# Kernel optimization log

Hardware: AMD Instinct MI355X
Metric: run time of the kernel (lower is better)

## Reference

```python
import jax, jax.numpy as jnp
import numpy as np
import math

VOCAB, D, L, H, DFF, S, B = 32000, 1024, 6, 16, 4096, 512, 4
DK = D // H
EPS = 1e-6


def layernorm(x, g, b):
    # Faithful to source: divides by (std + eps), std is population std (unbiased=False)
    mu = jnp.mean(x, axis=-1, keepdims=True)
    std = jnp.sqrt(jnp.mean((x - mu) ** 2, axis=-1, keepdims=True))
    return g * (x - mu) / (std + EPS) + b


def setup_inputs() -> dict:
    key = jax.random.key(0)
    ks = jax.random.split(key, 12)
    s = 0.02
    inp = {
        "tokens": jax.random.randint(ks[0], (B, S), 0, VOCAB, dtype=jnp.int32),
        "tok_emb": jax.random.normal(ks[1], (VOCAB, D), jnp.float32) * s,
        "pos_emb": jax.random.normal(ks[2], (1, S, D), jnp.float32) * s,
        # per-layer stacked params [L, ...]
        "Wq": jax.random.normal(ks[3], (L, D, D), jnp.float32) * s,
        "bq": jnp.zeros((L, D), jnp.float32),
        "Wk": jax.random.normal(ks[4], (L, D, D), jnp.float32) * s,
        "bk": jnp.zeros((L, D), jnp.float32),
        "Wv": jax.random.normal(ks[5], (L, D, D), jnp.float32) * s,
        "bv": jnp.zeros((L, D), jnp.float32),
        "Wo": jax.random.normal(ks[6], (L, D, D), jnp.float32) * s,
        "bo": jnp.zeros((L, D), jnp.float32),
        "g1": jnp.ones((L, D), jnp.float32),
        "be1": jnp.zeros((L, D), jnp.float32),
        "W1": jax.random.normal(ks[7], (L, D, DFF), jnp.float32) * s,
        "bf1": jnp.zeros((L, DFF), jnp.float32),
        "W2": jax.random.normal(ks[8], (L, DFF, D), jnp.float32) * s,
        "bf2": jnp.zeros((L, D), jnp.float32),
        "g2": jnp.ones((L, D), jnp.float32),
        "be2": jnp.zeros((L, D), jnp.float32),
        "gf": jnp.ones((D,), jnp.float32),
        "bf": jnp.zeros((D,), jnp.float32),
    }
    return inp


def gpt_forward(tokens, tok_emb, pos_emb, Wq, bq, Wk, bk, Wv, bv, Wo, bo,
                g1, be1, W1, bf1, W2, bf2, g2, be2, gf, bf):
    seq = tokens.shape[1]
    x = tok_emb[tokens] * math.sqrt(D) + pos_emb[:, :seq, :]  # [B,S,D]
    causal = jnp.tril(jnp.ones((seq, seq), bool))  # [S,S]

    def block(x, p):
        wq, bq_, wk, bk_, wv, bv_, wo, bo_, g1_, be1_, w1, bf1_, w2, bf2_, g2_, be2_ = p
        h = layernorm(x, g1_, be1_)
        q = (h @ wq + bq_).reshape(B, seq, H, DK).transpose(0, 2, 1, 3)  # [B,H,S,DK]
        k = (h @ wk + bk_).reshape(B, seq, H, DK).transpose(0, 2, 1, 3)
        v = (h @ wv + bv_).reshape(B, seq, H, DK).transpose(0, 2, 1, 3)
        scores = jnp.einsum("bhqd,bhkd->bhqk", q, k) / math.sqrt(DK)
        scores = jnp.where(causal, scores, -1e9)
        p_attn = jax.nn.softmax(scores, axis=-1)
        attn = jnp.einsum("bhqk,bhkd->bhqd", p_attn, v)
        attn = attn.transpose(0, 2, 1, 3).reshape(B, seq, D)
        x = x + (attn @ wo + bo_)
        h2 = layernorm(x, g2_, be2_)
        ff = jnp.maximum(h2 @ w1 + bf1_, 0.0) @ w2 + bf2_
        return x + ff, None

    params = (Wq, bq, Wk, bk, Wv, bv, Wo, bo, g1, be1, W1, bf1, W2, bf2, g2, be2)
    x, _ = jax.lax.scan(block, x, params)
    x = layernorm(x, gf, bf)
    logits = x @ tok_emb.T  # tied head, no bias
    return logits


def reference(tokens, tok_emb, pos_emb, Wq, bq, Wk, bk, Wv, bv, Wo, bo,
              g1, be1, W1, bf1, W2, bf2, g2, be2, gf, bf):
    return gpt_forward(tokens, tok_emb, pos_emb, Wq, bq, Wk, bk, Wv, bv, Wo, bo,
                       g1, be1, W1, bf1, W2, bf2, g2, be2, gf, bf)
```

## Files before the change

kernel.cpp:

```cpp
#include <hip/hip_runtime.h>

#define TOKENS 2048
#define DM 1024
#define NHEAD 16
#define DH 64
#define SEQL 512
#define NBATCH 4
#define DFFN 4096
#define NLAYER 6
#define NVOCAB 32000

typedef short short8 __attribute__((ext_vector_type(8)));
typedef short short4v __attribute__((ext_vector_type(4)));
typedef float floatx4 __attribute__((ext_vector_type(4)));

#define FLAG_RELU 1
#define FLAG_OUTBF16 2

#define AS1 __attribute__((address_space(1)))
#define AS3 __attribute__((address_space(3)))

__device__ __forceinline__ float bf2f(short s) {
  unsigned u = ((unsigned)(unsigned short)s) << 16;
  return __builtin_bit_cast(float, u);
}
__device__ __forceinline__ short f2bf(float f) {
  unsigned u = __builtin_bit_cast(unsigned, f);
  u = (u + 0x7FFFu + ((u >> 16) & 1u)) >> 16;
  return (short)(unsigned short)u;
}

template<int N> __device__ __forceinline__ void wait_vm() {
  if constexpr (N == 0)      asm volatile("s_waitcnt vmcnt(0)" ::: "memory");
  else if constexpr (N == 3) asm volatile("s_waitcnt vmcnt(3)" ::: "memory");
  else if constexpr (N == 4) asm volatile("s_waitcnt vmcnt(4)" ::: "memory");
  else if constexpr (N == 6) asm volatile("s_waitcnt vmcnt(6)" ::: "memory");
  else if constexpr (N == 8) asm volatile("s_waitcnt vmcnt(8)" ::: "memory");
  else static_assert(N == 0, "unsupported vmcnt");
}

template<int BM, int BN, int WR, int WC, int BK>
__global__ __launch_bounds__(256) void gemm_db(
    const short* __restrict__ A, const short* __restrict__ Bt, void* __restrict__ Cv,
    const float* __restrict__ bias, const float* __restrict__ resid,
    int K, int lda, int ldb, int ldc, float alpha, int flags)
{
  constexpr int FI = BM / WR / 16;
  constexpr int FJ = BN / WC / 16;
  constexpr int RPI = (BK == 64) ? 32 : 64;
  constexpr int NST = BM / RPI + BN / RPI;
  __shared__ short As[2][BM * BK];
  __shared__ short Bs[2][BN * BK];

  const int gy = gridDim.y;
  int lin = blockIdx.x + gridDim.x * blockIdx.y;
  const int nwg = gridDim.x * gy;
  if ((nwg & 7) == 0) { const int cpx = nwg >> 3; lin = (lin & 7) * cpx + (lin >> 3); }
  const int row0 = (lin % gy) * BM, col0 = (lin / gy) * BN;

  const int tid = threadIdx.x;
  const int lane = tid & 63;
  const int wid = tid >> 6;
  const int wr = wid / WC, wc = wid % WC;
  const int lc = lane & 15, g = lane >> 4;
  const int sr = (BK == 64) ? (tid >> 3) : (tid >> 2);
  const int sc = (BK == 64) ? (tid & 7) : (tid & 3);
  const int swz_s = (BK == 64) ? (sr & 7) : ((sr >> 1) & 3);
  const int scs = (sc ^ swz_s) * 8;

  floatx4 acc[FI][FJ];
  #pragma unroll
  for (int i = 0; i < FI; ++i)
    #pragma unroll
    for (int j = 0; j < FJ; ++j)
      acc[i][j] = (floatx4){0.f, 0.f, 0.f, 0.f};

  auto stage = [&](int k0, int b) {
    char* ad = (char*)As[b];
    char* bd = (char*)Bs[b];
    #pragma unroll
    for (int it = 0; it < BM / RPI; ++it) {
      const short* src = A + (long)(row0 + it * RPI + sr) * lda + k0 + scs;
      __builtin_amdgcn_global_load_lds((const AS1 void*)src,
          (AS3 void*)(ad + it * 4096 + tid * 16), 16, 0, 0);
    }
    #pragma unroll
    for (int it = 0; it < BN / RPI; ++it) {
      const short* src = Bt + (long)(col0 + it * RPI + sr) * ldb + k0 + scs;
      __builtin_amdgcn_global_load_lds((const AS1 void*)src,
          (AS3 void*)(bd + it * 4096 + tid * 16), 16, 0, 0);
    }
  };

  const int NT = K / BK;
  stage(0, 0);
  int cb = 0;
  for (int t = 0; t < NT; ++t) {
    __builtin_amdgcn_s_barrier();
    __builtin_amdgcn_sched_barrier(0);
    if (t + 1 < NT) {
      stage((t + 1) * BK, cb ^ 1);
      wait_vm<NST>();
    } else {
      wait_vm<0>();
    }
    __builtin_amdgcn_sched_barrier(0);

    const short* as = As[cb];
    const short* bs = Bs[cb];
    if constexpr (BK == 64) {
      short8 fa[FI][2], fb[FJ][2];
      #pragma unroll
      for (int i = 0; i < FI; ++i) {
        const int r = wr * (BM / WR) + i * 16 + lc;
        fa[i][0] = *(const short8*)&as[r * 64 + ((g ^ (r & 7)) * 8)];
        fa[i][1] = *(const short8*)&as[r * 64 + (((4 + g) ^ (r & 7)) * 8)];
      }
      #pragma unroll
      for (int j = 0; j < FJ; ++j) {
        const int r = wc * (BN / WC) + j * 16 + lc;
        fb[j][0] = *(const short8*)&bs[r * 64 + ((g ^ (r & 7)) * 8)];
        fb[j][1] = *(const short8*)&bs[r * 64 + (((4 + g) ^ (r & 7)) * 8)];
      }
      #pragma unroll
      for (int i = 0; i < FI; ++i)
        #pragma unroll
        for (int j = 0; j < FJ; ++j) {
          acc[i][j] = __builtin_amdgcn_mfma_f32_16x16x32_bf16(fa[i][0], fb[j][0], acc[i][j], 0, 0, 0);
          acc[i][j] = __builtin_amdgcn_mfma_f32_16x16x32_bf16(fa[i][1], fb[j][1], acc[i][j], 0, 0, 0);
        }
    } else {
      short8 fa[FI], fb[FJ];
      #pragma unroll
      for (int i = 0; i < FI; ++i) {
        const int r = wr * (BM / WR) + i * 16 + lc;
        fa[i] = *(const short8*)&as[r * 32 + ((g ^ ((r >> 1) & 3)) * 8)];
      }
      #pragma unroll
      for (int j = 0; j < FJ; ++j) {
        const int r = wc * (BN / WC) + j * 16 + lc;
        fb[j] = *(const short8*)&bs[r * 32 + ((g ^ ((r >> 1) & 3)) * 8)];
      }
      #pragma unroll
      for (int i = 0; i < FI; ++i)
        #pragma unroll
        for (int j = 0; j < FJ; ++j)
          acc[i][j] = __builtin_amdgcn_mfma_f32_16x16x32_bf16(fa[i], fb[j], acc[i][j], 0, 0, 0);
    }
    cb ^= 1;
  }

  const bool relu = flags & FLAG_RELU;
  const bool obf  = flags & FLAG_OUTBF16;
  float* Cf = (float*)Cv;
  short* Cb = (short*)Cv;
  #pragma unroll
  for (int i = 0; i < FI; ++i) {
    int orow = row0 + wr * (BM / WR) + i * 16 + g * 4;
    #pragma unroll
    for (int j = 0; j < FJ; ++j) {
      int ocol = col0 + wc * (BN / WC) + j * 16 + lc;
      #pragma unroll
      for (int t = 0; t < 4; ++t) {
        long off = (long)(orow + t) * ldc + ocol;
        float v = alpha * acc[i][j][t];
        if (bias)  v += bias[ocol];
        if (resid) v += resid[off];
        if (relu)  v = fmaxf(v, 0.f);
        if (obf) Cb[off] = f2bf(v); else Cf[off] = v;
      }
    }
  }
}

template<int BM, int BN, int WR, int WC, int BK>
static inline void launch_gemm(hipStream_t st, const short* A, const short* Bt, void* C,
    const float* bias, const float* resid, int M, int N, int K,
    int lda, int ldb, int ldc, float alpha, int flags)
{
  dim3 grid(N / BN, M / BM, 1), blk(256);
  gemm_db<BM, BN, WR, WC, BK><<<grid, blk, 0, st>>>(A, Bt, C, bias, resid,
                                                    K, lda, ldb, ldc, alpha, flags);
}

__global__ __launch_bounds__(512, 2) void gemm256p(
    const short* __restrict__ A, const short* __restrict__ Bt, float* __restrict__ C,
    int K, int lda, int ldb, int ldc)
{
  __shared__ short As[2][2][128 * 64];
  __shared__ short Bs[2][4][64 * 64];

  const int gy = gridDim.y;
  int lin = blockIdx.x + gridDim.x * blockIdx.y;
  const int nwg = gridDim.x * gy;
  if ((nwg & 7) == 0) { const int cpx = nwg >> 3; lin = (lin & 7) * cpx + (lin >> 3); }
  const int row0 = (lin % gy) * 256, col0 = (lin / gy) * 256;

  const int tid = threadIdx.x;
  const int lane = tid & 63;
  const int w = tid >> 6;
  const int wr = w >> 2, wc = w & 3;
  const int lc = lane & 15, g = lane >> 4;
  const int sr = tid >> 3;
  const int sc = tid & 7;
  const int scs = (sc ^ (sr & 7)) * 8;

  floatx4 acc[8][4];
  #pragma unroll
  for (int i = 0; i < 8; ++i)
    #pragma unroll
    for (int j = 0; j < 4; ++j)
      acc[i][j] = (floatx4){0.f, 0.f, 0.f, 0.f};

  auto stageA = [&](int k0, int b, int h) {
    #pragma unroll
    for (int it = 0; it < 2; ++it) {
      const int r = h * 128 + it * 64 + sr;
      const short* src = A + (long)(row0 + r) * lda + k0 + scs;
      __builtin_amdgcn_global_load_lds((const AS1 void*)src,
          (AS3 void*)((char*)&As[b][h][0] + it * 8192 + tid * 16), 16, 0, 0);
    }
  };
  auto stageBq = [&](int k0, int b, int q) {
    const short* src = Bt + (long)(col0 + q * 64 + sr) * ldb + k0 + scs;
    __builtin_amdgcn_global_load_lds((const AS1 void*)src,
        (AS3 void*)((char*)&Bs[b][q][0] + tid * 16), 16, 0, 0);
  };
  auto rdA = [&](int b, int sub, short8 fa[4][2]) {
    const short* base = &As[b][wr][0];
    #pragma unroll
    for (int i = 0; i < 4; ++i) {
      const int r = sub * 64 + i * 16 + lc;
      fa[i][0] = *(const short8*)&base[r * 64 + ((g ^ (r & 7)) * 8)];
      fa[i][1] = *(const short8*)&base[r * 64 + (((4 + g) ^ (r & 7)) * 8)];
    }
  };
  auto rdB = [&](int b, int sub, short8 fb[2][2]) {
    const short* base = &Bs[b][wc][0];
    #pragma unroll
    for (int j = 0; j < 2; ++j) {
      const int r = sub * 32 + j * 16 + lc;
      fb[j][0] = *(const short8*)&base[r * 64 + ((g ^ (r & 7)) * 8)];
      fb[j][1] = *(const short8*)&base[r * 64 + (((4 + g) ^ (r & 7)) * 8)];
    }
  };
  auto mm = [&](short8 fa[4][2], short8 fb[2][2], int io, int jo) {
    #pragma unroll
    for (int i = 0; i < 4; ++i)
      #pragma unroll
      for (int j = 0; j < 2; ++j) {
        floatx4 c = acc[io + i][jo + j];
        c = __builtin_amdgcn_mfma_f32_16x16x32_bf16(fa[i][0], fb[j][0], c, 0, 0, 0);
        c = __builtin_amdgcn_mfma_f32_16x16x32_bf16(fa[i][1], fb[j][1], c, 0, 0, 0);
        acc[io + i][jo + j] = c;
      }
  };

#define PH_SYNC() \
    __builtin_amdgcn_s_barrier(); \
    asm volatile("s_waitcnt lgkmcnt(0)" ::: "memory"); \
    __builtin_amdgcn_sched_barrier(0); \
    __builtin_amdgcn_s_setprio(1);
#define PH_END() \
    __builtin_amdgcn_s_setprio(0); \
    __builtin_amdgcn_s_barrier();

  const int NT = K >> 6;
  stageA(0, 0, 0); stageA(0, 0, 1);
  stageBq(0, 0, 0); stageBq(0, 0, 1); stageBq(0, 0, 2); stageBq(0, 0, 3);
  stageA(64, 1, 0); stageA(64, 1, 1);
  wait_vm<4>();
  __builtin_amdgcn_s_barrier();

  for (int t = 0; t < NT; ++t) {
    const int b = t & 1;
    const int nk = (t + 1) << 6;
    short8 fa[4][2], fb0[2][2], fb1[2][2];
    rdA(b, 0, fa); rdB(b, 0, fb0);
    if (t + 1 < NT) { stageBq(nk, b ^ 1, 0); stageBq(nk, b ^ 1, 1); }
    PH_SYNC();
    mm(fa, fb0, 0, 0);
    PH_END();
    rdB(b, 1, fb1);
    if (t + 1 < NT) { stageBq(nk, b ^ 1, 2); stageBq(nk, b ^ 1, 3); }
    PH_SYNC();
    mm(fa, fb1, 0, 2);
    PH_END();
    rdA(b, 1, fa);
    PH_SYNC();
    mm(fa, fb1, 4, 2);
    PH_END();
    if (t + 2 < NT) {
      stageA((t + 2) << 6, b, 0); stageA((t + 2) << 6, b, 1);
      wait_vm<4>();
    } else {
      wait_vm<0>();
    }
    __builtin_amdgcn_sched_barrier(0);
    __builtin_amdgcn_s_barrier();
    __builtin_amdgcn_s_setprio(1);
    mm(fa, fb0, 4, 0);
    PH_END();
  }
#undef PH_SYNC
#undef PH_END

  #pragma unroll
  for (int i = 0; i < 8; ++i) {
    int orow = row0 + wr * 128 + i * 16 + g * 4;
    #pragma unroll
    for (int j = 0; j < 4; ++j) {
      int ocol = col0 + wc * 64 + j * 16 + lc;
      #pragma unroll
      for (int t = 0; t < 4; ++t)
        C[(long)(orow + t) * ldc + ocol] = acc[i][j][t];
    }
  }
}

__global__ __launch_bounds__(256) void flash_attn(
    const short* __restrict__ qkv, const short* __restrict__ Vt,
    short* __restrict__ attn)
{
  const int qt = blockIdx.x;
  const int bh = blockIdx.y;
  const int b = bh >> 4, h = bh & 15;
  const int row0 = qt * 64;

  __shared__ short Kt[64 * 64];
  __shared__ short Vtl[64 * 64];
  __shared__ short Pt[4 * 16 * 64];

  const int tid = threadIdx.x;
  const int lane = tid & 63;
  const int wid = tid >> 6;
  const int lc = lane & 15, g = lane >> 4;

  short8 qf[2];
  {
    const short* qp = qkv + (long)(b * SEQL + row0 + wid * 16 + lc) * 3072 + h * DH;
    qf[0] = *(const short8*)(qp + g * 8);
    qf[1] = *(const short8*)(qp + 32 + g * 8);
  }

  floatx4 o[4];
  float m[4], l[4];
  #pragma unroll
  for (int j = 0; j < 4; ++j) o[j] = (floatx4){0.f, 0.f, 0.f, 0.f};
  #pragma unroll
  for (int t = 0; t < 4; ++t) { m[t] = -3e38f; l[t] = 0.f; }

  for (int kv0 = 0; kv0 <= row0; kv0 += 64) {
    #pragma unroll
    for (int i = 0; i < 2; ++i) {
      const int idx = i * 256 + tid;
      const int r = idx >> 3, cc = idx & 7;
      const int sw = cc ^ (r & 7);
      const short* ks = qkv + (long)(b * SEQL + kv0 + r) * 3072 + 1024 + h * DH + sw * 8;
      __builtin_amdgcn_global_load_lds((const AS1 void*)ks,
          (AS3 void*)((char*)Kt + (i * 256 + wid * 64) * 16), 16, 0, 0);
      const short* vs = Vt + (long)bh * DH * SEQL + (long)r * SEQL + kv0 + sw * 8;
      __builtin_amdgcn_global_load_lds((const AS1 void*)vs,
          (AS3 void*)((char*)Vtl + (i * 256 + wid * 64) * 16), 16, 0, 0);
    }
    __syncthreads();

    floatx4 s[4];
    #pragma unroll
    for (int j = 0; j < 4; ++j) s[j] = (floatx4){0.f, 0.f, 0.f, 0.f};
    #pragma unroll
    for (int ks_ = 0; ks_ < 2; ++ks_) {
      #pragma unroll
      for (int j = 0; j < 4; ++j) {
        const int row = j * 16 + lc;
        const short8 kf = *(const short8*)&Kt[row * 64 + ((ks_ * 4 + g) ^ (row & 7)) * 8];
        s[j] = __builtin_amdgcn_mfma_f32_16x16x32_bf16(qf[ks_], kf, s[j], 0, 0, 0);
      }
    }

    const bool diag = (kv0 == row0);
    float p[4][4], rmax[4], rsum[4];
    #pragma unroll
    for (int t = 0; t < 4; ++t) rmax[t] = -3e38f;
    #pragma unroll
    for (int j = 0; j < 4; ++j)
      #pragma unroll
      for (int t = 0; t < 4; ++t) {
        float sv = s[j][t] * 0.125f;
        if (diag && (j * 16 + lc) > (wid * 16 + g * 4 + t)) sv = -3e38f;
        p[j][t] = sv;
        rmax[t] = fmaxf(rmax[t], sv);
      }
    #pragma unroll
    for (int t = 0; t < 4; ++t) {
      #pragma unroll
      for (int mk = 1; mk < 16; mk <<= 1)
        rmax[t] = fmaxf(rmax[t], __shfl_xor(rmax[t], mk));
    }
    bool need = (rmax[0] > m[0] + 8.f) || (rmax[1] > m[1] + 8.f) ||
                (rmax[2] > m[2] + 8.f) || (rmax[3] > m[3] + 8.f);
    if (__any(need)) {
      float fs[4];
      #pragma unroll
      for (int t = 0; t < 4; ++t) {
        float mn = fmaxf(m[t], rmax[t]);
        fs[t] = __expf(m[t] - mn);
        m[t] = mn;
        l[t] *= fs[t];
      }
      #pragma unroll
      for (int j = 0; j < 4; ++j) {
        o[j][0] *= fs[0]; o[j][1] *= fs[1]; o[j][2] *= fs[2]; o[j][3] *= fs[3];
      }
    }
    #pragma unroll
    for (int j = 0; j < 4; ++j)
      #pragma unroll
      for (int t = 0; t < 4; ++t)
        p[j][t] = __expf(p[j][t] - m[t]);
    #pragma unroll
    for (int t = 0; t < 4; ++t) {
      rsum[t] = p[0][t] + p[1][t] + p[2][t] + p[3][t];
      #pragma unroll
      for (int mk = 1; mk < 16; mk <<= 1)
        rsum[t] += __shfl_xor(rsum[t], mk);
      l[t] += rsum[t];
    }
    #pragma unroll
    for (int j = 0; j < 4; ++j)
      #pragma unroll
      for (int t = 0; t < 4; ++t) {
        const int r = g * 4 + t;
        const int col = j * 16 + lc;
        Pt[wid * 1024 + r * 64 + (((col >> 3) ^ (r & 7)) * 8) + (col & 7)] = f2bf(p[j][t]);
      }
    __syncthreads();

    #pragma unroll
    for (int ks_ = 0; ks_ < 2; ++ks_) {
      const short8 pf = *(const short8*)&Pt[wid * 1024 + lc * 64 + ((ks_ * 4 + g) ^ (lc & 7)) * 8];
      #pragma unroll
      for (int j = 0; j < 4; ++j) {
        const int row = j * 16 + lc;
        const short8 vf = *(const short8*)&Vtl[row * 64 + ((ks_ * 4 + g) ^ (row & 7)) * 8];
        o[j] = __builtin_amdgcn_mfma_f32_16x16x32_bf16(pf, vf, o[j], 0, 0, 0);
      }
    }
    __syncthreads();
  }

  float linv[4];
  #pragma unroll
  for (int t = 0; t < 4; ++t) linv[t] = 1.f / l[t];
  #pragma unroll
  for (int j = 0; j < 4; ++j)
    #pragma unroll
    for (int t = 0; t < 4; ++t) {
      const long row = (long)(b * SEQL + row0 + wid * 16 + g * 4 + t);
      attn[row * DM + h * DH + j * 16 + lc] = f2bf(o[j][t] * linv[t]);
    }
}

__global__ __launch_bounds__(256) void ln_bf16(const float* __restrict__ x,
    const float* __restrict__ gg, const float* __restrict__ bb, short* __restrict__ out)
{
  int row = blockIdx.x;
  const float4 u = ((const float4*)(x + (long)row * DM))[threadIdx.x];
  float s  = u.x + u.y + u.z + u.w;
  float sq = u.x * u.x + u.y * u.y + u.z * u.z + u.w * u.w;
  #pragma unroll
  for (int o = 32; o; o >>= 1) { s += __shfl_xor(s, o); sq += __shfl_xor(sq, o); }
  __shared__ float red[8];
  int lane = threadIdx.x & 63, wid = threadIdx.x >> 6;
  if (lane == 0) { red[wid] = s; red[4 + wid] = sq; }
  __syncthreads();
  s  = red[0] + red[1] + red[2] + red[3];
  sq = red[4] + red[5] + red[6] + red[7];
  float mu  = s * (1.f / DM);
  float var = fmaxf(sq * (1.f / DM) - mu * mu, 0.f);
  float inv = 1.f / (sqrtf(var) + 1e-6f);
  int c = threadIdx.x * 4;
  const float4 gv = ((const float4*)gg)[threadIdx.x];
  const float4 bv = ((const float4*)bb)[threadIdx.x];
  short4v o;
  o[0] = f2bf((u.x - mu) * inv * gv.x + bv.x);
  o[1] = f2bf((u.y - mu) * inv * gv.y + bv.y);
  o[2] = f2bf((u.z - mu) * inv * gv.z + bv.z);
  o[3] = f2bf((u.w - mu) * inv * gv.w + bv.w);
  *(short4v*)(out + (long)row * DM + c) = o;
}

__global__ __launch_bounds__(256) void embed_k(const int* __restrict__ toks,
    const float* __restrict__ emb, const float* __restrict__ pos, float* __restrict__ x)
{
  int row = blockIdx.x;
  int s = row & (SEQL - 1);
  long tk = toks[row];
  const float4 e = ((const float4*)(emb + tk * DM))[threadIdx.x];
  const float4 p = ((const float4*)(pos + (long)s * DM))[threadIdx.x];
  float4 o;
  o.x = e.x * 32.f + p.x; o.y = e.y * 32.f + p.y;
  o.z = e.z * 32.f + p.z; o.w = e.w * 32.f + p.w;
  ((float4*)(x + (long)row * DM))[threadIdx.x] = o;
}

__global__ void wtrans(const float* __restrict__ W, short* __restrict__ Wt,
                       int K, int N, long zsout)
{
  __shared__ float tile[32][33];
  const long lo = (long)blockIdx.z * K * N;
  const long oo = (long)blockIdx.z * zsout;
  int n0 = blockIdx.x * 32, k0 = blockIdx.y * 32;
  int tx = threadIdx.x, ty = threadIdx.y;
  #pragma unroll
  for (int i = 0; i < 4; ++i)
    tile[ty + i * 8][tx] = W[lo + (long)(k0 + ty + i * 8) * N + n0 + tx];
  __syncthreads();
  #pragma unroll
  for (int i = 0; i < 4; ++i)
    Wt[oo + (long)(n0 + ty + i * 8) * K + k0 + tx] = f2bf(tile[tx][ty + i * 8]);
}

__global__ __launch_bounds__(256) void conv_bf16(const float* __restrict__ in,
                                                 short* __restrict__ out)
{
  long i = ((long)blockIdx.x * 256 + threadIdx.x) * 8;
  float4 a = *(const float4*)(in + i);
  float4 b = *(const float4*)(in + i + 4);
  short8 o;
  o[0] = f2bf(a.x); o[1] = f2bf(a.y); o[2] = f2bf(a.z); o[3] = f2bf(a.w);
  o[4] = f2bf(b.x); o[5] = f2bf(b.y); o[6] = f2bf(b.z); o[7] = f2bf(b.w);
  *(short8*)(out + i) = o;
}

__global__ void vtrans(const short* __restrict__ qkv, short* __restrict__ Vt)
{
  __shared__ short tile[32][33];
  int bh = blockIdx.z;
  int b = bh >> 4, h = bh & 15;
  int s0 = blockIdx.x * 32, d0 = blockIdx.y * 32;
  int tx = threadIdx.x, ty = threadIdx.y;
  #pragma unroll
  for (int i = 0; i < 4; ++i)
    tile[ty + i * 8][tx] =
        qkv[((long)(b * SEQL + s0 + ty + i * 8)) * 3072 + 2048 + h * DH + d0 + tx];
  __syncthreads();
  #pragma unroll
  for (int i = 0; i < 4; ++i)
    Vt[((long)(bh * DH + d0 + ty + i * 8)) * SEQL + s0 + tx] = tile[tx][ty + i * 8];
}

__global__ void bias_cat(const float* __restrict__ bq, const float* __restrict__ bk,
                         const float* __restrict__ bv, float* __restrict__ out)
{
  int l = blockIdx.y;
  int i = blockIdx.x * 256 + threadIdx.x;
  float v = (i < 1024) ? bq[l * 1024 + i]
          : (i < 2048) ? bk[l * 1024 + i - 1024]
                       : bv[l * 1024 + i - 2048];
  out[(long)l * 3072 + i] = v;
}

extern "C" void kernel_launch(void* const* d_in, const int* in_sizes, int n_in,
                              void* d_out, int out_size, void* d_ws, size_t ws_size,
                              hipStream_t stream)
{
  (void)in_sizes; (void)n_in; (void)out_size;
  const int*   toks = (const int*)  d_in[0];
  const float* temb = (const float*)d_in[1];
  const float* pemb = (const float*)d_in[2];
  const float* Wq  = (const float*)d_in[3];  const float* bq  = (const float*)d_in[4];
  const float* Wk  = (const float*)d_in[5];  const float* bk  = (const float*)d_in[6];
  const float* Wv  = (const float*)d_in[7];  const float* bv  = (const float*)d_in[8];
  const float* Wo  = (const float*)d_in[9];  const float* bo  = (const float*)d_in[10];
  const float* g1  = (const float*)d_in[11]; const float* be1 = (const float*)d_in[12];
  const float* W1  = (const float*)d_in[13]; const float* bf1 = (const float*)d_in[14];
  const float* W2  = (const float*)d_in[15]; const float* bf2 = (const float*)d_in[16];
  const float* g2  = (const float*)d_in[17]; const float* be2 = (const float*)d_in[18];
  const float* gf  = (const float*)d_in[19]; const float* bfb = (const float*)d_in[20];

  char* p = (char*)d_ws;
  auto carve = [&](size_t bytes) -> char* {
    char* r = p;
    p += (bytes + 255) & ~(size_t)255;
    return r;
  };
  short* h     = (short*)carve((size_t)TOKENS * DM * 2);
  char*  uni   = p;
  short* tembb = (short*)uni;
  short* Wqkvt = (short*)carve((size_t)NLAYER * 3072 * DM * 2);
  short* Wot   = (short*)carve((size_t)NLAYER * DM * DM * 2);
  short* W1t   = (short*)carve((size_t)NLAYER * DM * DFFN * 2);
  short* W2t   = (short*)carve((size_t)NLAYER * DM * DFFN * 2);
  float* x     = (float*)carve((size_t)TOKENS * DM * 4);
  short* qkv   = (short*)carve((size_t)TOKENS * 3072 * 2);
  short* attn  = (short*)carve((size_t)TOKENS * DM * 2);
  short* Vt    = (short*)carve((size_t)NBATCH * NHEAD * DH * SEQL * 2);
  short* ffb   = (short*)carve((size_t)TOKENS * DFFN * 2);
  float* bqkv  = (float*)carve((size_t)NLAYER * 3072 * 4);
  size_t used = (size_t)(p - (char*)d_ws);
  size_t need_t = (size_t)(uni - (char*)d_ws) + (size_t)NVOCAB * DM * 2;
  if (used > ws_size || need_t > ws_size) return;

  dim3 tb(32, 8);

  embed_k<<<TOKENS, 256, 0, stream>>>(toks, temb, pemb, x);
  bias_cat<<<dim3(12, NLAYER), 256, 0, stream>>>(bq, bk, bv, bqkv);
  wtrans<<<dim3(DM / 32, DM / 32, NLAYER), tb, 0, stream>>>(Wq, Wqkvt, DM, DM, 3072L * DM);
  wtrans<<<dim3(DM / 32, DM / 32, NLAYER), tb, 0, stream>>>(Wk, Wqkvt + (size_t)DM * DM, DM, DM, 3072L * DM);
  wtrans<<<dim3(DM / 32, DM / 32, NLAYER), tb, 0, stream>>>(Wv, Wqkvt + (size_t)2 * DM * DM, DM, DM, 3072L * DM);
  wtrans<<<dim3(DM / 32, DM / 32, NLAYER), tb, 0, stream>>>(Wo, Wot, DM, DM, (long)DM * DM);
  wtrans<<<dim3(DFFN / 32, DM / 32, NLAYER), tb, 0, stream>>>(W1, W1t, DM, DFFN, (long)DM * DFFN);
  wtrans<<<dim3(DM / 32, DFFN / 32, NLAYER), tb, 0, stream>>>(W2, W2t, DFFN, DM, (long)DM * DFFN);

  for (int l = 0; l < NLAYER; ++l) {
    const size_t wqkv = (size_t)l * 3072 * DM;
    const size_t wdd  = (size_t)l * DM * DM;
    const size_t wdf  = (size_t)l * DM * DFFN;
    ln_bf16<<<TOKENS, 256, 0, stream>>>(x, g1 + l * DM, be1 + l * DM, h);
    launch_gemm<64, 128, 1, 4, 64>(stream, h, Wqkvt + wqkv, qkv, bqkv + (size_t)l * 3072,
        nullptr, TOKENS, 3072, DM, DM, DM, 3072, 1.f, FLAG_OUTBF16);
    vtrans<<<dim3(SEQL / 32, DH / 32, NBATCH * NHEAD), tb, 0, stream>>>(qkv, Vt);
    flash_attn<<<dim3(SEQL / 64, NBATCH * NHEAD), 256, 0, stream>>>(qkv, Vt, attn);
    launch_gemm<64, 64, 2, 2, 64>(stream, attn, Wot + wdd, x, bo + l * DM, x,
        TOKENS, DM, DM, DM, DM, DM, 1.f, 0);
    ln_bf16<<<TOKENS, 256, 0, stream>>>(x, g2 + l * DM, be2 + l * DM, h);
    launch_gemm<64, 128, 1, 4, 64>(stream, h, W1t + wdf, ffb, bf1 + l * DFFN, nullptr,
        TOKENS, DFFN, DM, DM, DM, DFFN, 1.f, FLAG_OUTBF16 | FLAG_RELU);
    launch_gemm<64, 64, 2, 2, 64>(stream, ffb, W2t + wdf, x, bf2 + l * DM, x,
        TOKENS, DM, DFFN, DFFN, DFFN, DM, 1.f, 0);
  }
  ln_bf16<<<TOKENS, 256, 0, stream>>>(x, gf, bfb, h);
  conv_bf16<<<(NVOCAB * DM) / (256 * 8), 256, 0, stream>>>(temb, tembb);
  {
    dim3 grid(NVOCAB / 256, TOKENS / 256, 1), blk(512);
    gemm256p<<<grid, blk, 0, stream>>>(h, tembb, (float*)d_out, DM, DM, DM, NVOCAB);
  }
}
```

Measured before the change: 1.434 ms.

## Merge weight transposes, drop bias concat kernel, retile FFN1 GEMM to 128x128

Measured after the change: 1.358 ms. 1.06x faster.

```diff
diff --git a/kernel.cpp b/kernel.cpp
--- a/kernel.cpp
+++ b/kernel.cpp
@@ -42,7 +42,8 @@
 template<int BM, int BN, int WR, int WC, int BK>
 __global__ __launch_bounds__(256) void gemm_db(
     const short* __restrict__ A, const short* __restrict__ Bt, void* __restrict__ Cv,
-    const float* __restrict__ bias, const float* __restrict__ resid,
+    const float* __restrict__ bias, const float* __restrict__ biask,
+    const float* __restrict__ biasv, const float* __restrict__ resid,
     int K, int lda, int ldb, int ldc, float alpha, int flags)
 {
   constexpr int FI = BM / WR / 16;
@@ -160,11 +161,17 @@
     #pragma unroll
     for (int j = 0; j < FJ; ++j) {
       int ocol = col0 + wc * (BN / WC) + j * 16 + lc;
+      const float* bp = bias;
+      int bc = ocol;
+      if (biask) {
+        if (ocol >= 2048)      { bp = biasv; bc = ocol - 2048; }
+        else if (ocol >= 1024) { bp = biask; bc = ocol - 1024; }
+      }
       #pragma unroll
       for (int t = 0; t < 4; ++t) {
         long off = (long)(orow + t) * ldc + ocol;
         float v = alpha * acc[i][j][t];
-        if (bias)  v += bias[ocol];
+        if (bp)    v += bp[bc];
         if (resid) v += resid[off];
         if (relu)  v = fmaxf(v, 0.f);
         if (obf) Cb[off] = f2bf(v); else Cf[off] = v;
@@ -175,11 +182,11 @@
 
 template<int BM, int BN, int WR, int WC, int BK>
 static inline void launch_gemm(hipStream_t st, const short* A, const short* Bt, void* C,
-    const float* bias, const float* resid, int M, int N, int K,
-    int lda, int ldb, int ldc, float alpha, int flags)
+    const float* bias, const float* biask, const float* biasv, const float* resid,
+    int M, int N, int K, int lda, int ldb, int ldc, float alpha, int flags)
 {
   dim3 grid(N / BN, M / BM, 1), blk(256);
-  gemm_db<BM, BN, WR, WC, BK><<<grid, blk, 0, st>>>(A, Bt, C, bias, resid,
+  gemm_db<BM, BN, WR, WC, BK><<<grid, blk, 0, st>>>(A, Bt, C, bias, biask, biasv, resid,
                                                     K, lda, ldb, ldc, alpha, flags);
 }
 
@@ -504,13 +511,44 @@
   ((float4*)(x + (long)row * DM))[threadIdx.x] = o;
 }
 
-__global__ void wtrans(const float* __restrict__ W, short* __restrict__ Wt,
-                       int K, int N, long zsout)
+__global__ void wtrans4(const float* __restrict__ Wq, const float* __restrict__ Wk,
+                        const float* __restrict__ Wv, const float* __restrict__ Wo,
+                        short* __restrict__ Wqkvt, short* __restrict__ Wot)
 {
   __shared__ float tile[32][33];
-  const long lo = (long)blockIdx.z * K * N;
-  const long oo = (long)blockIdx.z * zsout;
+  const int z = blockIdx.z;
+  const int w = z / NLAYER, l = z % NLAYER;
+  const float* W = (w == 0) ? Wq : (w == 1) ? Wk : (w == 2) ? Wv : Wo;
+  const long lo = (long)l * DM * DM;
+  short* dst;
+  long oo;
+  if (w < 3) { dst = Wqkvt; oo = (long)l * 3072 * DM + (long)w * DM * DM; }
+  else       { dst = Wot;   oo = (long)l * DM * DM; }
   int n0 = blockIdx.x * 32, k0 = blockIdx.y * 32;
+  int tx = threadIdx.x, ty = threadIdx.y;
+  #pragma unroll
+  for (int i = 0; i < 4; ++i)
+    tile[ty + i * 8][tx] = W[lo + (long)(k0 + ty + i * 8) * DM + n0 + tx];
+  __syncthreads();
+  #pragma unroll
+  for (int i = 0; i < 4; ++i)
+    dst[oo + (long)(n0 + ty + i * 8) * DM + k0 + tx] = f2bf(tile[tx][ty + i * 8]);
+}
+
+__global__ void wtransF(const float* __restrict__ W1, const float* __restrict__ W2,
+                        short* __restrict__ W1t, short* __restrict__ W2t)
+{
+  __shared__ float tile[32][33];
+  const int z = blockIdx.z;
+  const int w = z / NLAYER, l = z % NLAYER;
+  const int K = w ? DFFN : DM;
+  const int N = w ? DM : DFFN;
+  const float* W = w ? W2 : W1;
+  short* dst = (w ? W2t : W1t);
+  const long lo = (long)l * DM * DFFN;
+  const long oo = (long)l * DM * DFFN;
+  int n0 = (w ? blockIdx.y : blockIdx.x) * 32;
+  int k0 = (w ? blockIdx.x : blockIdx.y) * 32;
   int tx = threadIdx.x, ty = threadIdx.y;
   #pragma unroll
   for (int i = 0; i < 4; ++i)
@@ -518,7 +556,7 @@
   __syncthreads();
   #pragma unroll
   for (int i = 0; i < 4; ++i)
-    Wt[oo + (long)(n0 + ty + i * 8) * K + k0 + tx] = f2bf(tile[tx][ty + i * 8]);
+    dst[oo + (long)(n0 + ty + i * 8) * K + k0 + tx] = f2bf(tile[tx][ty + i * 8]);
 }
 
 __global__ __launch_bounds__(256) void conv_bf16(const float* __restrict__ in,
@@ -548,17 +586,6 @@
   #pragma unroll
   for (int i = 0; i < 4; ++i)
     Vt[((long)(bh * DH + d0 + ty + i * 8)) * SEQL + s0 + tx] = tile[tx][ty + i * 8];
-}
-
-__global__ void bias_cat(const float* __restrict__ bq, const float* __restrict__ bk,
-                         const float* __restrict__ bv, float* __restrict__ out)
-{
-  int l = blockIdx.y;
-  int i = blockIdx.x * 256 + threadIdx.x;
-  float v = (i < 1024) ? bq[l * 1024 + i]
-          : (i < 2048) ? bk[l * 1024 + i - 1024]
-                       : bv[l * 1024 + i - 2048];
-  out[(long)l * 3072 + i] = v;
 }
 
 extern "C" void kernel_launch(void* const* d_in, const int* in_sizes, int n_in,
@@ -597,7 +624,6 @@
   short* attn  = (short*)carve((size_t)TOKENS * DM * 2);
   short* Vt    = (short*)carve((size_t)NBATCH * NHEAD * DH * SEQL * 2);
   short* ffb   = (short*)carve((size_t)TOKENS * DFFN * 2);
-  float* bqkv  = (float*)carve((size_t)NLAYER * 3072 * 4);
   size_t used = (size_t)(p - (char*)d_ws);
   size_t need_t = (size_t)(uni - (char*)d_ws) + (size_t)NVOCAB * DM * 2;
   if (used > ws_size || need_t > ws_size) return;
@@ -605,29 +631,28 @@
   dim3 tb(32, 8);
 
   embed_k<<<TOKENS, 256, 0, stream>>>(toks, temb, pemb, x);
-  bias_cat<<<dim3(12, NLAYER), 256, 0, stream>>>(bq, bk, bv, bqkv);
-  wtrans<<<dim3(DM / 32, DM / 32, NLAYER), tb, 0, stream>>>(Wq, Wqkvt, DM, DM, 3072L * DM);
-  wtrans<<<dim3(DM / 32, DM / 32, NLAYER), tb, 0, stream>>>(Wk, Wqkvt + (size_t)DM * DM, DM, DM, 3072L * DM);
-  wtrans<<<dim3(DM / 32, DM / 32, NLAYER), tb, 0, stream>>>(Wv, Wqkvt + (size_t)2 * DM * DM, DM, DM, 3072L * DM);
-  wtrans<<<dim3(DM / 32, DM / 32, NLAYER), tb, 0, stream>>>(Wo, Wot, DM, DM, (long)DM * DM);
-  wtrans<<<dim3(DFFN / 32, DM / 32, NLAYER), tb, 0, stream>>>(W1, W1t, DM, DFFN, (long)DM * DFFN);
-  wtrans<<<dim3(DM / 32, DFFN / 32, NLAYER), tb, 0, stream>>>(W2, W2t, DFFN, DM, (long)DM * DFFN);
+  wtrans4<<<dim3(DM / 32, DM / 32, 4 * NLAYER), tb, 0, stream>>>(Wq, Wk, Wv, Wo, Wqkvt, Wot);
+  wtransF<<<dim3(DFFN / 32, DM / 32, 2 * NLAYER), tb, 0, stream>>>(W1, W2, W1t, W2t);
 
   for (int l = 0; l < NLAYER; ++l) {
     const size_t wqkv = (size_t)l * 3072 * DM;
     const size_t wdd  = (size_t)l * DM * DM;
     const size_t wdf  = (size_t)l * DM * DFFN;
     ln_bf16<<<TOKENS, 256, 0, stream>>>(x, g1 + l * DM, be1 + l * DM, h);
-    launch_gemm<64, 128, 1, 4, 64>(stream, h, Wqkvt + wqkv, qkv, bqkv + (size_t)l * 3072,
-        nullptr, TOKENS, 3072, DM, DM, DM, 3072, 1.f, FLAG_OUTBF16);
+    launch_gemm<64, 128, 1, 4, 64>(stream, h, Wqkvt + wqkv, qkv,
+        bq + l * DM, bk + l * DM, bv + l * DM, nullptr,
+        TOKENS, 3072, DM, DM, DM, 3072, 1.f, FLAG_OUTBF16);
     vtrans<<<dim3(SEQL / 32, DH / 32, NBATCH * NHEAD), tb, 0, stream>>>(qkv, Vt);
     flash_attn<<<dim3(SEQL / 64, NBATCH * NHEAD), 256, 0, stream>>>(qkv, Vt, attn);
-    launch_gemm<64, 64, 2, 2, 64>(stream, attn, Wot + wdd, x, bo + l * DM, x,
+    launch_gemm<64, 64, 2, 2, 64>(stream, attn, Wot + wdd, x,
+        bo + l * DM, nullptr, nullptr, x,
         TOKENS, DM, DM, DM, DM, DM, 1.f, 0);
     ln_bf16<<<TOKENS, 256, 0, stream>>>(x, g2 + l * DM, be2 + l * DM, h);
-    launch_gemm<64, 128, 1, 4, 64>(stream, h, W1t + wdf, ffb, bf1 + l * DFFN, nullptr,
+    launch_gemm<128, 128, 2, 2, 64>(stream, h, W1t + wdf, ffb,
+        bf1 + l * DFFN, nullptr, nullptr, nullptr,
         TOKENS, DFFN, DM, DM, DM, DFFN, 1.f, FLAG_OUTBF16 | FLAG_RELU);
-    launch_gemm<64, 64, 2, 2, 64>(stream, ffb, W2t + wdf, x, bf2 + l * DM, x,
+    launch_gemm<64, 64, 2, 2, 64>(stream, ffb, W2t + wdf, x,
+        bf2 + l * DM, nullptr, nullptr, x,
         TOKENS, DM, DFFN, DFFN, DFFN, DM, 1.f, 0);
   }
   ln_bf16<<<TOKENS, 256, 0, stream>>>(x, gf, bfb, h);
```
